# Performance work log

Measured on AMD Instinct MI355X. Metric: run time of the kernel, lower is better.

The kernel has to match this reference:

```python
import jax, jax.numpy as jnp
import numpy as np

B, T = 2048, 8
IN_DIM, OUT_DIM, E = 1024, 4096, 12


def setup_inputs() -> dict:
    key = jax.random.key(0)
    k = jax.random.split(key, 6)
    s = 1.0 / np.sqrt(IN_DIM)
    sg = 1.0 / np.sqrt(OUT_DIM)
    return {
        "x": jax.random.normal(k[0], (B, 1, IN_DIM), dtype=jnp.float32),
        "t": jax.random.normal(k[1], (B, T, OUT_DIM), dtype=jnp.float32),
        "W": jax.random.uniform(k[2], (E, IN_DIM, OUT_DIM), dtype=jnp.float32, minval=-s, maxval=s),
        "b": jax.random.uniform(k[3], (E, OUT_DIM), dtype=jnp.float32, minval=-s, maxval=s),
        "Wg": jax.random.uniform(k[4], (OUT_DIM, E), dtype=jnp.float32, minval=-sg, maxval=sg),
        "bg": jax.random.uniform(k[5], (E,), dtype=jnp.float32, minval=-sg, maxval=sg),
    }


def reference(x, t, W, b, Wg, bg):
    # x: [B,1,in], t: [B,T,out], W: [E,in,out], b: [E,out], Wg: [out,E], bg: [E]
    x_flat = x[:, 0, :]                                   # [B,in]
    t_mean = t.mean(axis=1)                               # [B,out]
    gate_logits = t_mean @ Wg + bg                        # [B,E]
    top1 = jnp.argmax(gate_logits, axis=-1)               # [B]
    # Dense per-expert linear, then select the top-1 expert's row per token.
    all_out = jnp.einsum('bi,eio->beo', x_flat, W) + b    # [B,E,out]
    out = all_out[jnp.arange(x.shape[0]), top1]           # [B,out]
    return out[:, None, :]                                # [B,1,out]
```

## Files before the change

### kernel.cpp

```cpp
#include <hip/hip_runtime.h>
#include <hip/hip_bf16.h>

#define B_ROWS  2048
#define T_DIM   8
#define IN_DIM  1024
#define OUT_DIM 4096
#define NE      12

#define M_TILE 128
#define N_TILE 128
#define K_STEP 32
#define NSTEP  (IN_DIM / K_STEP)

typedef __attribute__((ext_vector_type(8))) short short8;
typedef __attribute__((ext_vector_type(4))) float f32x4;

union S8U { short8 s; unsigned u[4]; };

__device__ __forceinline__ unsigned cvt2(float a, float b) {
  __hip_bfloat162 h = __float22bfloat162_rn(make_float2(a, b));
  union { __hip_bfloat162 h; unsigned u; } c; c.h = h;
  return c.u;
}

__device__ __forceinline__ void barrier_lgkm() {
  asm volatile("s_waitcnt lgkmcnt(0)" ::: "memory");
  __builtin_amdgcn_s_barrier();
}

__global__ __launch_bounds__(256) void wg_transpose(
    const float* __restrict__ Wg, float* __restrict__ wgt)
{
  const int c = blockIdx.x * 256 + threadIdx.x;
  #pragma unroll
  for (int e = 0; e < NE; ++e)
    wgt[(size_t)e * OUT_DIM + c] = Wg[(size_t)c * NE + e];
}

__global__ __launch_bounds__(256) void gate_kernel(
    const float* __restrict__ t, const float* __restrict__ wgt,
    const float* __restrict__ bg, int* __restrict__ counts,
    int* __restrict__ rowlist)
{
  const int b   = blockIdx.x;
  const int tid = threadIdx.x;
  const float* tb = t + (size_t)b * T_DIM * OUT_DIM;

  float4 m[4];
  #pragma unroll
  for (int it = 0; it < 4; ++it) {
    const int c = (tid + it * 256) * 4;
    float4 s = make_float4(0.f, 0.f, 0.f, 0.f);
    #pragma unroll
    for (int tt = 0; tt < T_DIM; ++tt) {
      const float4 v = *(const float4*)(tb + (size_t)tt * OUT_DIM + c);
      s.x += v.x; s.y += v.y; s.z += v.z; s.w += v.w;
    }
    m[it] = make_float4(s.x * 0.125f, s.y * 0.125f, s.z * 0.125f, s.w * 0.125f);
  }

  float part[NE];
  #pragma unroll
  for (int e = 0; e < NE; ++e) {
    float acc = 0.f;
    #pragma unroll
    for (int it = 0; it < 4; ++it) {
      const int c = (tid + it * 256) * 4;
      const float4 w = *(const float4*)(wgt + (size_t)e * OUT_DIM + c);
      acc += m[it].x * w.x; acc += m[it].y * w.y;
      acc += m[it].z * w.z; acc += m[it].w * w.w;
    }
    part[e] = acc;
  }

  double d[NE];
  #pragma unroll
  for (int e = 0; e < NE; ++e) d[e] = (double)part[e];
  #pragma unroll
  for (int off = 32; off > 0; off >>= 1) {
    #pragma unroll
    for (int e = 0; e < NE; ++e) d[e] += __shfl_down(d[e], off, 64);
  }

  __shared__ double wsred[4][NE];
  const int lane = tid & 63, wave = tid >> 6;
  if (lane == 0) {
    #pragma unroll
    for (int e = 0; e < NE; ++e) wsred[wave][e] = d[e];
  }
  __syncthreads();

  if (tid == 0) {
    double best = -1e300; int bi = 0;
    #pragma unroll
    for (int e = 0; e < NE; ++e) {
      const double v = wsred[0][e] + wsred[1][e] + wsred[2][e] + wsred[3][e] + (double)bg[e];
      if (v > best) { best = v; bi = e; }
    }
    const int pos = atomicAdd(&counts[bi], 1);
    rowlist[bi * B_ROWS + pos] = b;
  }
}

__global__ __launch_bounds__(256) void gate_fallback(
    const float* __restrict__ t, const float* __restrict__ Wg,
    const float* __restrict__ bg, int* __restrict__ counts,
    int* __restrict__ rowlist)
{
  const int b   = blockIdx.x;
  const int tid = threadIdx.x;
  const float* tb = t + (size_t)b * T_DIM * OUT_DIM;

  float part[NE];
  #pragma unroll
  for (int e = 0; e < NE; ++e) part[e] = 0.f;
  #pragma unroll
  for (int it = 0; it < 4; ++it) {
    const int c = (tid + it * 256) * 4;
    float4 s = make_float4(0.f, 0.f, 0.f, 0.f);
    #pragma unroll
    for (int tt = 0; tt < T_DIM; ++tt) {
      const float4 v = *(const float4*)(tb + (size_t)tt * OUT_DIM + c);
      s.x += v.x; s.y += v.y; s.z += v.z; s.w += v.w;
    }
    const float mm[4] = { s.x * 0.125f, s.y * 0.125f, s.z * 0.125f, s.w * 0.125f };
    #pragma unroll
    for (int j = 0; j < 4; ++j) {
      const float* wg = Wg + (size_t)(c + j) * NE;
      #pragma unroll
      for (int e = 0; e < NE; ++e) part[e] += mm[j] * wg[e];
    }
  }
  double d[NE];
  #pragma unroll
  for (int e = 0; e < NE; ++e) d[e] = (double)part[e];
  #pragma unroll
  for (int off = 32; off > 0; off >>= 1) {
    #pragma unroll
    for (int e = 0; e < NE; ++e) d[e] += __shfl_down(d[e], off, 64);
  }
  __shared__ double wsred[4][NE];
  const int lane = tid & 63, wave = tid >> 6;
  if (lane == 0) {
    #pragma unroll
    for (int e = 0; e < NE; ++e) wsred[wave][e] = d[e];
  }
  __syncthreads();
  if (tid == 0) {
    double best = -1e300; int bi = 0;
    #pragma unroll
    for (int e = 0; e < NE; ++e) {
      const double v = wsred[0][e] + wsred[1][e] + wsred[2][e] + wsred[3][e] + (double)bg[e];
      if (v > best) { best = v; bi = e; }
    }
    const int pos = atomicAdd(&counts[bi], 1);
    rowlist[bi * B_ROWS + pos] = b;
  }
}

__global__ __launch_bounds__(256) void expert_gemm(
    const float* __restrict__ x, const float* __restrict__ W,
    const float* __restrict__ bias, const int* __restrict__ counts,
    const int* __restrict__ rowlist, float* __restrict__ out)
{
  const int e    = blockIdx.z;
  const int cnt  = counts[e];
  const int row0 = blockIdx.y * M_TILE;
  if (row0 >= cnt) return;
  const int c0   = blockIdx.x * N_TILE;
  const int* rl  = rowlist + e * B_ROWS;

  __shared__ short8 xa[2][512];
  __shared__ short8 wb[2][512];

  const int tid  = threadIdx.x;
  const int lane = tid & 63;
  const int wave = tid >> 6;

  const int sg  = (tid >> 4) & 3;
  const int slr = tid & 15;
  const int smb = tid >> 6;

  int arow0, arow1;
  {
    const int g0 = row0 + smb * 16 + slr;
    const int g1 = row0 + (smb + 4) * 16 + slr;
    arow0 = rl[g0 < cnt ? g0 : cnt - 1];
    arow1 = rl[g1 < cnt ? g1 : cnt - 1];
  }
  const float* xp0 = x + (size_t)arow0 * IN_DIM + sg * 8;
  const float* xp1 = x + (size_t)arow1 * IN_DIM + sg * 8;
  const float* wp  = W + (size_t)e * IN_DIM * OUT_DIM
                       + (size_t)(sg * 8) * OUT_DIM + c0 + smb * 16 + slr;

  const int wm = (wave >> 1) * 64;
  const int wn = (wave & 1) * 64;
  const int abase = (wave >> 1) * 256;
  const int bbase = (wave & 1) * 256;

  f32x4 acc[4][4];
  #pragma unroll
  for (int m = 0; m < 4; ++m)
    #pragma unroll
    for (int n = 0; n < 4; ++n)
      #pragma unroll
      for (int q = 0; q < 4; ++q) acc[m][n][q] = 0.f;

  float4 a0lo, a0hi, a1lo, a1hi;
  float w0[8], w1[8];

#define ISSUE_LOADS(K)                                                  \
  {                                                                     \
    a0lo = *(const float4*)(xp0 + (K));                                 \
    a0hi = *(const float4*)(xp0 + (K) + 4);                             \
    a1lo = *(const float4*)(xp1 + (K));                                 \
    a1hi = *(const float4*)(xp1 + (K) + 4);                             \
    const float* p = wp + (size_t)(K) * OUT_DIM;                        \
    _Pragma("unroll")                                                   \
    for (int j = 0; j < 8; ++j) {                                       \
      w0[j] = p[(size_t)j * OUT_DIM];                                   \
      w1[j] = p[(size_t)j * OUT_DIM + 64];                              \
    }                                                                   \
  }

  ISSUE_LOADS(0);

  for (int it = 0; it < NSTEP; ++it) {
    S8U av0, av1, bv0, bv1;
    av0.u[0] = cvt2(a0lo.x, a0lo.y); av0.u[1] = cvt2(a0lo.z, a0lo.w);
    av0.u[2] = cvt2(a0hi.x, a0hi.y); av0.u[3] = cvt2(a0hi.z, a0hi.w);
    av1.u[0] = cvt2(a1lo.x, a1lo.y); av1.u[1] = cvt2(a1lo.z, a1lo.w);
    av1.u[2] = cvt2(a1hi.x, a1hi.y); av1.u[3] = cvt2(a1hi.z, a1hi.w);
    #pragma unroll
    for (int q = 0; q < 4; ++q) {
      bv0.u[q] = cvt2(w0[2 * q], w0[2 * q + 1]);
      bv1.u[q] = cvt2(w1[2 * q], w1[2 * q + 1]);
    }

    if (it + 1 < NSTEP) ISSUE_LOADS((it + 1) * K_STEP);

    const int buf = it & 1;
    xa[buf][tid]       = av0.s;
    xa[buf][tid + 256] = av1.s;
    wb[buf][tid]       = bv0.s;
    wb[buf][tid + 256] = bv1.s;
    barrier_lgkm();

    short8 af[4], bf[4];
    #pragma unroll
    for (int m = 0; m < 4; ++m) af[m] = xa[buf][abase + m * 64 + lane];
    #pragma unroll
    for (int n = 0; n < 4; ++n) bf[n] = wb[buf][bbase + n * 64 + lane];
    #pragma unroll
    for (int m = 0; m < 4; ++m)
      #pragma unroll
      for (int n = 0; n < 4; ++n)
        acc[m][n] = __builtin_amdgcn_mfma_f32_16x16x32_bf16(af[m], bf[n], acc[m][n], 0, 0, 0);
  }
#undef ISSUE_LOADS

  const int lr = lane & 15;
  const int lq = (lane >> 4) * 4;
  float bcol[4];
  #pragma unroll
  for (int n = 0; n < 4; ++n)
    bcol[n] = bias[e * OUT_DIM + c0 + wn + n * 16 + lr];

  #pragma unroll
  for (int m = 0; m < 4; ++m) {
    #pragma unroll
    for (int r = 0; r < 4; ++r) {
      const int gidx = row0 + wm + m * 16 + lq + r;
      if (gidx >= cnt) continue;
      const int grow = rl[gidx];
      float* orow = out + (size_t)grow * OUT_DIM;
      #pragma unroll
      for (int n = 0; n < 4; ++n) {
        const int col = c0 + wn + n * 16 + lr;
        orow[col] = acc[m][n][r] + bcol[n];
      }
    }
  }
}

extern "C" void kernel_launch(void* const* d_in, const int* in_sizes, int n_in,
                              void* d_out, int out_size, void* d_ws, size_t ws_size,
                              hipStream_t stream) {
  (void)in_sizes; (void)n_in; (void)out_size;
  const float* x  = (const float*)d_in[0];
  const float* t  = (const float*)d_in[1];
  const float* W  = (const float*)d_in[2];
  const float* bb = (const float*)d_in[3];
  const float* Wg = (const float*)d_in[4];
  const float* bg = (const float*)d_in[5];
  float* out = (float*)d_out;

  int*   counts  = (int*)d_ws;
  int*   rowlist = (int*)d_ws + 16;
  float* wgt     = (float*)((char*)d_ws + 64 + NE * B_ROWS * 4);
  const size_t need = 64 + (size_t)NE * B_ROWS * 4 + (size_t)NE * OUT_DIM * 4;

  hipMemsetAsync(counts, 0, 16 * sizeof(int), stream);
  if (ws_size >= need) {
    wg_transpose<<<OUT_DIM / 256, 256, 0, stream>>>(Wg, wgt);
    gate_kernel<<<B_ROWS, 256, 0, stream>>>(t, wgt, bg, counts, rowlist);
  } else {
    gate_fallback<<<B_ROWS, 256, 0, stream>>>(t, Wg, bg, counts, rowlist);
  }

  dim3 grid(OUT_DIM / N_TILE, (B_ROWS + M_TILE - 1) / M_TILE, NE);
  expert_gemm<<<grid, 256, 0, stream>>>(x, W, bb, counts, rowlist, out);
}
```

Measured before the change: 172.2 us.

## Split expert GEMM along K with atomic accumulation and bias pre-initialization

The expert GEMM is split four ways along the input dimension, so the grid has four times as many blocks, each running a quarter of the K loop. Partial sums are combined with float atomicAdd into the output. The output is first initialized with the selected expert's bias inside the gate kernel. The aim is more parallelism and better latency hiding in a GEMM that has few active tiles per expert. The cost is four atomic passes over the output, an extra full output write in the gate kernel, more per-block prologue overhead, and non-deterministic summation order.

```diff
diff --git a/kernel.cpp b/kernel.cpp
--- a/kernel.cpp
+++ b/kernel.cpp
@@ -11,6 +11,8 @@
 #define N_TILE 128
 #define K_STEP 32
 #define NSTEP  (IN_DIM / K_STEP)
+#define KSPLIT 4
+#define CSTEPS (NSTEP / KSPLIT)
 
 typedef __attribute__((ext_vector_type(8))) short short8;
 typedef __attribute__((ext_vector_type(4))) float f32x4;
@@ -39,8 +41,9 @@
 
 __global__ __launch_bounds__(256) void gate_kernel(
     const float* __restrict__ t, const float* __restrict__ wgt,
-    const float* __restrict__ bg, int* __restrict__ counts,
-    int* __restrict__ rowlist)
+    const float* __restrict__ bg, const float* __restrict__ bias,
+    int* __restrict__ counts, int* __restrict__ rowlist,
+    float* __restrict__ out)
 {
   const int b   = blockIdx.x;
   const int tid = threadIdx.x;
@@ -83,6 +86,7 @@
   }
 
   __shared__ double wsred[4][NE];
+  __shared__ int s_bi;
   const int lane = tid & 63, wave = tid >> 6;
   if (lane == 0) {
     #pragma unroll
@@ -99,13 +103,25 @@
     }
     const int pos = atomicAdd(&counts[bi], 1);
     rowlist[bi * B_ROWS + pos] = b;
+    s_bi = bi;
+  }
+  __syncthreads();
+
+  const int bi = s_bi;
+  const float* brow = bias + (size_t)bi * OUT_DIM;
+  float* orow = out + (size_t)b * OUT_DIM;
+  #pragma unroll
+  for (int it = 0; it < 4; ++it) {
+    const int c = (tid + it * 256) * 4;
+    *(float4*)(orow + c) = *(const float4*)(brow + c);
   }
 }
 
 __global__ __launch_bounds__(256) void gate_fallback(
     const float* __restrict__ t, const float* __restrict__ Wg,
-    const float* __restrict__ bg, int* __restrict__ counts,
-    int* __restrict__ rowlist)
+    const float* __restrict__ bg, const float* __restrict__ bias,
+    int* __restrict__ counts, int* __restrict__ rowlist,
+    float* __restrict__ out)
 {
   const int b   = blockIdx.x;
   const int tid = threadIdx.x;
@@ -140,6 +156,7 @@
     for (int e = 0; e < NE; ++e) d[e] += __shfl_down(d[e], off, 64);
   }
   __shared__ double wsred[4][NE];
+  __shared__ int s_bi;
   const int lane = tid & 63, wave = tid >> 6;
   if (lane == 0) {
     #pragma unroll
@@ -155,15 +172,26 @@
     }
     const int pos = atomicAdd(&counts[bi], 1);
     rowlist[bi * B_ROWS + pos] = b;
+    s_bi = bi;
+  }
+  __syncthreads();
+  const int bi = s_bi;
+  const float* brow = bias + (size_t)bi * OUT_DIM;
+  float* orow = out + (size_t)b * OUT_DIM;
+  #pragma unroll
+  for (int it = 0; it < 4; ++it) {
+    const int c = (tid + it * 256) * 4;
+    *(float4*)(orow + c) = *(const float4*)(brow + c);
   }
 }
 
 __global__ __launch_bounds__(256) void expert_gemm(
     const float* __restrict__ x, const float* __restrict__ W,
-    const float* __restrict__ bias, const int* __restrict__ counts,
-    const int* __restrict__ rowlist, float* __restrict__ out)
+    const int* __restrict__ counts, const int* __restrict__ rowlist,
+    float* __restrict__ out)
 {
-  const int e    = blockIdx.z;
+  const int e    = blockIdx.z / KSPLIT;
+  const int kc   = blockIdx.z % KSPLIT;
   const int cnt  = counts[e];
   const int row0 = blockIdx.y * M_TILE;
   if (row0 >= cnt) return;
@@ -223,9 +251,10 @@
     }                                                                   \
   }
 
-  ISSUE_LOADS(0);
-
-  for (int it = 0; it < NSTEP; ++it) {
+  const int it0 = kc * CSTEPS;
+  ISSUE_LOADS(it0 * K_STEP);
+
+  for (int it = it0; it < it0 + CSTEPS; ++it) {
     S8U av0, av1, bv0, bv1;
     av0.u[0] = cvt2(a0lo.x, a0lo.y); av0.u[1] = cvt2(a0lo.z, a0lo.w);
     av0.u[2] = cvt2(a0hi.x, a0hi.y); av0.u[3] = cvt2(a0hi.z, a0hi.w);
@@ -237,7 +266,7 @@
       bv1.u[q] = cvt2(w1[2 * q], w1[2 * q + 1]);
     }
 
-    if (it + 1 < NSTEP) ISSUE_LOADS((it + 1) * K_STEP);
+    if (it + 1 < it0 + CSTEPS) ISSUE_LOADS((it + 1) * K_STEP);
 
     const int buf = it & 1;
     xa[buf][tid]       = av0.s;
@@ -261,11 +290,6 @@
 
   const int lr = lane & 15;
   const int lq = (lane >> 4) * 4;
-  float bcol[4];
-  #pragma unroll
-  for (int n = 0; n < 4; ++n)
-    bcol[n] = bias[e * OUT_DIM + c0 + wn + n * 16 + lr];
-
   #pragma unroll
   for (int m = 0; m < 4; ++m) {
     #pragma unroll
@@ -277,7 +301,7 @@
       #pragma unroll
       for (int n = 0; n < 4; ++n) {
         const int col = c0 + wn + n * 16 + lr;
-        orow[col] = acc[m][n][r] + bcol[n];
+        atomicAdd(&orow[col], acc[m][n][r]);
       }
     }
   }
@@ -303,11 +327,11 @@
   hipMemsetAsync(counts, 0, 16 * sizeof(int), stream);
   if (ws_size >= need) {
     wg_transpose<<<OUT_DIM / 256, 256, 0, stream>>>(Wg, wgt);
-    gate_kernel<<<B_ROWS, 256, 0, stream>>>(t, wgt, bg, counts, rowlist);
+    gate_kernel<<<B_ROWS, 256, 0, stream>>>(t, wgt, bg, bb, counts, rowlist, out);
   } else {
-    gate_fallback<<<B_ROWS, 256, 0, stream>>>(t, Wg, bg, counts, rowlist);
-  }
-
-  dim3 grid(OUT_DIM / N_TILE, (B_ROWS + M_TILE - 1) / M_TILE, NE);
-  expert_gemm<<<grid, 256, 0, stream>>>(x, W, bb, counts, rowlist, out);
-}
+    gate_fallback<<<B_ROWS, 256, 0, stream>>>(t, Wg, bg, bb, counts, rowlist, out);
+  }
+
+  dim3 grid(OUT_DIM / N_TILE, (B_ROWS + M_TILE - 1) / M_TILE, NE * KSPLIT);
+  expert_gemm<<<grid, 256, 0, stream>>>(x, W, counts, rowlist, out);
+}
```

Measured after the change: 222.8 us. 1.29x slower.

## Double expert GEMM M tile to 256 and remap blocks for XCD locality

Applied to the files above, without the earlier changes.

Raises the expert GEMM row tile from 128 to 256. Each wave now computes a 64x128 output slab (acc 4x8), so every weight tile loaded from global is reused across twice as many token rows, which cuts W traffic. It also remaps the flattened block index so that neighbouring hardware dispatch slots map to the same expert and column range, aiming at better L2 sharing across XCDs. The cost is more accumulator registers (128 floats per lane) and therefore lower occupancy, plus coarser tail waste when an expert's token count is not a multiple of 256.

```diff
diff --git a/kernel.cpp b/kernel.cpp
--- a/kernel.cpp
+++ b/kernel.cpp
@@ -7,7 +7,7 @@
 #define OUT_DIM 4096
 #define NE      12
 
-#define M_TILE 128
+#define M_TILE 256
 #define N_TILE 128
 #define K_STEP 32
 #define NSTEP  (IN_DIM / K_STEP)
@@ -163,14 +163,16 @@
     const float* __restrict__ bias, const int* __restrict__ counts,
     const int* __restrict__ rowlist, float* __restrict__ out)
 {
-  const int e    = blockIdx.z;
+  const int bx = blockIdx.x;
+  const int gw = (bx & 7) * 48 + (bx >> 3) + 4 * blockIdx.z;
+  const int e  = gw >> 5;
+  const int c0 = (gw & 31) * N_TILE;
   const int cnt  = counts[e];
   const int row0 = blockIdx.y * M_TILE;
   if (row0 >= cnt) return;
-  const int c0   = blockIdx.x * N_TILE;
   const int* rl  = rowlist + e * B_ROWS;
 
-  __shared__ short8 xa[2][512];
+  __shared__ short8 xa[2][1024];
   __shared__ short8 wb[2][512];
 
   const int tid  = threadIdx.x;
@@ -181,40 +183,35 @@
   const int slr = tid & 15;
   const int smb = tid >> 6;
 
-  int arow0, arow1;
-  {
-    const int g0 = row0 + smb * 16 + slr;
-    const int g1 = row0 + (smb + 4) * 16 + slr;
-    arow0 = rl[g0 < cnt ? g0 : cnt - 1];
-    arow1 = rl[g1 < cnt ? g1 : cnt - 1];
-  }
-  const float* xp0 = x + (size_t)arow0 * IN_DIM + sg * 8;
-  const float* xp1 = x + (size_t)arow1 * IN_DIM + sg * 8;
-  const float* wp  = W + (size_t)e * IN_DIM * OUT_DIM
-                       + (size_t)(sg * 8) * OUT_DIM + c0 + smb * 16 + slr;
-
-  const int wm = (wave >> 1) * 64;
-  const int wn = (wave & 1) * 64;
-  const int abase = (wave >> 1) * 256;
-  const int bbase = (wave & 1) * 256;
-
-  f32x4 acc[4][4];
+  const float* xp[4];
+  #pragma unroll
+  for (int i = 0; i < 4; ++i) {
+    const int g = row0 + (smb + 4 * i) * 16 + slr;
+    xp[i] = x + (size_t)rl[g < cnt ? g : cnt - 1] * IN_DIM + sg * 8;
+  }
+  const float* wp = W + (size_t)e * IN_DIM * OUT_DIM
+                      + (size_t)(sg * 8) * OUT_DIM + c0 + smb * 16 + slr;
+
+  const int wm    = wave * 64;
+  const int abase = wave * 256;
+
+  f32x4 acc[4][8];
   #pragma unroll
   for (int m = 0; m < 4; ++m)
     #pragma unroll
-    for (int n = 0; n < 4; ++n)
+    for (int n = 0; n < 8; ++n)
       #pragma unroll
       for (int q = 0; q < 4; ++q) acc[m][n][q] = 0.f;
 
-  float4 a0lo, a0hi, a1lo, a1hi;
+  float4 axl0, axh0, axl1, axh1, axl2, axh2, axl3, axh3;
   float w0[8], w1[8];
 
 #define ISSUE_LOADS(K)                                                  \
   {                                                                     \
-    a0lo = *(const float4*)(xp0 + (K));                                 \
-    a0hi = *(const float4*)(xp0 + (K) + 4);                             \
-    a1lo = *(const float4*)(xp1 + (K));                                 \
-    a1hi = *(const float4*)(xp1 + (K) + 4);                             \
+    axl0 = *(const float4*)(xp[0] + (K)); axh0 = *(const float4*)(xp[0] + (K) + 4); \
+    axl1 = *(const float4*)(xp[1] + (K)); axh1 = *(const float4*)(xp[1] + (K) + 4); \
+    axl2 = *(const float4*)(xp[2] + (K)); axh2 = *(const float4*)(xp[2] + (K) + 4); \
+    axl3 = *(const float4*)(xp[3] + (K)); axh3 = *(const float4*)(xp[3] + (K) + 4); \
     const float* p = wp + (size_t)(K) * OUT_DIM;                        \
     _Pragma("unroll")                                                   \
     for (int j = 0; j < 8; ++j) {                                       \
@@ -226,11 +223,15 @@
   ISSUE_LOADS(0);
 
   for (int it = 0; it < NSTEP; ++it) {
-    S8U av0, av1, bv0, bv1;
-    av0.u[0] = cvt2(a0lo.x, a0lo.y); av0.u[1] = cvt2(a0lo.z, a0lo.w);
-    av0.u[2] = cvt2(a0hi.x, a0hi.y); av0.u[3] = cvt2(a0hi.z, a0hi.w);
-    av1.u[0] = cvt2(a1lo.x, a1lo.y); av1.u[1] = cvt2(a1lo.z, a1lo.w);
-    av1.u[2] = cvt2(a1hi.x, a1hi.y); av1.u[3] = cvt2(a1hi.z, a1hi.w);
+    S8U av0, av1, av2, av3, bv0, bv1;
+    av0.u[0] = cvt2(axl0.x, axl0.y); av0.u[1] = cvt2(axl0.z, axl0.w);
+    av0.u[2] = cvt2(axh0.x, axh0.y); av0.u[3] = cvt2(axh0.z, axh0.w);
+    av1.u[0] = cvt2(axl1.x, axl1.y); av1.u[1] = cvt2(axl1.z, axl1.w);
+    av1.u[2] = cvt2(axh1.x, axh1.y); av1.u[3] = cvt2(axh1.z, axh1.w);
+    av2.u[0] = cvt2(axl2.x, axl2.y); av2.u[1] = cvt2(axl2.z, axl2.w);
+    av2.u[2] = cvt2(axh2.x, axh2.y); av2.u[3] = cvt2(axh2.z, axh2.w);
+    av3.u[0] = cvt2(axl3.x, axl3.y); av3.u[1] = cvt2(axl3.z, axl3.w);
+    av3.u[2] = cvt2(axh3.x, axh3.y); av3.u[3] = cvt2(axh3.z, axh3.w);
     #pragma unroll
     for (int q = 0; q < 4; ++q) {
       bv0.u[q] = cvt2(w0[2 * q], w0[2 * q + 1]);
@@ -242,29 +243,31 @@
     const int buf = it & 1;
     xa[buf][tid]       = av0.s;
     xa[buf][tid + 256] = av1.s;
+    xa[buf][tid + 512] = av2.s;
+    xa[buf][tid + 768] = av3.s;
     wb[buf][tid]       = bv0.s;
     wb[buf][tid + 256] = bv1.s;
     barrier_lgkm();
 
-    short8 af[4], bf[4];
+    short8 af[4], bf[8];
     #pragma unroll
     for (int m = 0; m < 4; ++m) af[m] = xa[buf][abase + m * 64 + lane];
     #pragma unroll
-    for (int n = 0; n < 4; ++n) bf[n] = wb[buf][bbase + n * 64 + lane];
+    for (int n = 0; n < 8; ++n) bf[n] = wb[buf][n * 64 + lane];
     #pragma unroll
     for (int m = 0; m < 4; ++m)
       #pragma unroll
-      for (int n = 0; n < 4; ++n)
+      for (int n = 0; n < 8; ++n)
         acc[m][n] = __builtin_amdgcn_mfma_f32_16x16x32_bf16(af[m], bf[n], acc[m][n], 0, 0, 0);
   }
 #undef ISSUE_LOADS
 
   const int lr = lane & 15;
   const int lq = (lane >> 4) * 4;
-  float bcol[4];
-  #pragma unroll
-  for (int n = 0; n < 4; ++n)
-    bcol[n] = bias[e * OUT_DIM + c0 + wn + n * 16 + lr];
+  float bcol[8];
+  #pragma unroll
+  for (int n = 0; n < 8; ++n)
+    bcol[n] = bias[e * OUT_DIM + c0 + n * 16 + lr];
 
   #pragma unroll
   for (int m = 0; m < 4; ++m) {
@@ -275,8 +278,8 @@
       const int grow = rl[gidx];
       float* orow = out + (size_t)grow * OUT_DIM;
       #pragma unroll
-      for (int n = 0; n < 4; ++n) {
-        const int col = c0 + wn + n * 16 + lr;
+      for (int n = 0; n < 8; ++n) {
+        const int col = c0 + n * 16 + lr;
         orow[col] = acc[m][n][r] + bcol[n];
       }
     }
@@ -308,6 +311,6 @@
     gate_fallback<<<B_ROWS, 256, 0, stream>>>(t, Wg, bg, counts, rowlist);
   }
 
-  dim3 grid(OUT_DIM / N_TILE, (B_ROWS + M_TILE - 1) / M_TILE, NE);
+  dim3 grid(OUT_DIM / N_TILE, B_ROWS / M_TILE, NE);
   expert_gemm<<<grid, 256, 0, stream>>>(x, W, bb, counts, rowlist, out);
 }
```

Measured after the change: 181.2 us. 1.05x slower.

## Shrink GEMM N tile to 64 and remap blocks for XCD-aware scheduling

Applied to the files above, without the earlier changes.

Halves the expert GEMM column tile from 128 to 64. Each wave now computes a 32x64 slice instead of 64x64, which cuts accumulator registers and shared memory so that up to four blocks can share a CU (launch_bounds 256,4). Blocks are flattened into a 1D work index with an interleave over groups of 8, likely so that blocks on the same XCD share the same expert and weights in L2. Pairs of row tiles go along x so that launch order favours low row tiles. Smaller tiles mean more x reloads per W byte and less MFMA reuse per LDS load, in exchange for better occupancy and load balance across the uneven expert counts.

```diff
diff --git a/kernel.cpp b/kernel.cpp
--- a/kernel.cpp
+++ b/kernel.cpp
@@ -8,9 +8,10 @@
 #define NE      12
 
 #define M_TILE 128
-#define N_TILE 128
+#define N_TILE 64
 #define K_STEP 32
 #define NSTEP  (IN_DIM / K_STEP)
+#define NWORK  (NE * (OUT_DIM / N_TILE) * 2)
 
 typedef __attribute__((ext_vector_type(8))) short short8;
 typedef __attribute__((ext_vector_type(4))) float f32x4;
@@ -158,20 +159,24 @@
   }
 }
 
-__global__ __launch_bounds__(256) void expert_gemm(
+__global__ __launch_bounds__(256, 4) void expert_gemm(
     const float* __restrict__ x, const float* __restrict__ W,
     const float* __restrict__ bias, const int* __restrict__ counts,
     const int* __restrict__ rowlist, float* __restrict__ out)
 {
-  const int e    = blockIdx.z;
+  const int bid = blockIdx.x;
+  const int wk  = (bid & 7) * (NWORK / 8) + (bid >> 3);
+  const int e   = wk >> 7;
+  const int rem = wk & 127;
+  const int c0  = (rem >> 1) * N_TILE;
+  const int rt  = rem & 1;
   const int cnt  = counts[e];
-  const int row0 = blockIdx.y * M_TILE;
+  const int row0 = (blockIdx.y * 2 + rt) * M_TILE;
   if (row0 >= cnt) return;
-  const int c0   = blockIdx.x * N_TILE;
   const int* rl  = rowlist + e * B_ROWS;
 
   __shared__ short8 xa[2][512];
-  __shared__ short8 wb[2][512];
+  __shared__ short8 wb[2][256];
 
   const int tid  = threadIdx.x;
   const int lane = tid & 63;
@@ -193,21 +198,16 @@
   const float* wp  = W + (size_t)e * IN_DIM * OUT_DIM
                        + (size_t)(sg * 8) * OUT_DIM + c0 + smb * 16 + slr;
 
-  const int wm = (wave >> 1) * 64;
-  const int wn = (wave & 1) * 64;
-  const int abase = (wave >> 1) * 256;
-  const int bbase = (wave & 1) * 256;
-
-  f32x4 acc[4][4];
-  #pragma unroll
-  for (int m = 0; m < 4; ++m)
+  f32x4 acc[2][4];
+  #pragma unroll
+  for (int m = 0; m < 2; ++m)
     #pragma unroll
     for (int n = 0; n < 4; ++n)
       #pragma unroll
       for (int q = 0; q < 4; ++q) acc[m][n][q] = 0.f;
 
   float4 a0lo, a0hi, a1lo, a1hi;
-  float w0[8], w1[8];
+  float w0[8];
 
 #define ISSUE_LOADS(K)                                                  \
   {                                                                     \
@@ -217,25 +217,20 @@
     a1hi = *(const float4*)(xp1 + (K) + 4);                             \
     const float* p = wp + (size_t)(K) * OUT_DIM;                        \
     _Pragma("unroll")                                                   \
-    for (int j = 0; j < 8; ++j) {                                       \
-      w0[j] = p[(size_t)j * OUT_DIM];                                   \
-      w1[j] = p[(size_t)j * OUT_DIM + 64];                              \
-    }                                                                   \
+    for (int j = 0; j < 8; ++j) w0[j] = p[(size_t)j * OUT_DIM];         \
   }
 
   ISSUE_LOADS(0);
 
   for (int it = 0; it < NSTEP; ++it) {
-    S8U av0, av1, bv0, bv1;
+    S8U av0, av1, bv0;
     av0.u[0] = cvt2(a0lo.x, a0lo.y); av0.u[1] = cvt2(a0lo.z, a0lo.w);
     av0.u[2] = cvt2(a0hi.x, a0hi.y); av0.u[3] = cvt2(a0hi.z, a0hi.w);
     av1.u[0] = cvt2(a1lo.x, a1lo.y); av1.u[1] = cvt2(a1lo.z, a1lo.w);
     av1.u[2] = cvt2(a1hi.x, a1hi.y); av1.u[3] = cvt2(a1hi.z, a1hi.w);
     #pragma unroll
-    for (int q = 0; q < 4; ++q) {
+    for (int q = 0; q < 4; ++q)
       bv0.u[q] = cvt2(w0[2 * q], w0[2 * q + 1]);
-      bv1.u[q] = cvt2(w1[2 * q], w1[2 * q + 1]);
-    }
 
     if (it + 1 < NSTEP) ISSUE_LOADS((it + 1) * K_STEP);
 
@@ -243,16 +238,17 @@
     xa[buf][tid]       = av0.s;
     xa[buf][tid + 256] = av1.s;
     wb[buf][tid]       = bv0.s;
-    wb[buf][tid + 256] = bv1.s;
     barrier_lgkm();
 
-    short8 af[4], bf[4];
-    #pragma unroll
-    for (int m = 0; m < 4; ++m) af[m] = xa[buf][abase + m * 64 + lane];
-    #pragma unroll
-    for (int n = 0; n < 4; ++n) bf[n] = wb[buf][bbase + n * 64 + lane];
-    #pragma unroll
-    for (int m = 0; m < 4; ++m)
+    short8 af[2], bf[4];
+    #pragma unroll
+    for (int m = 0; m < 2; ++m)
+      af[m] = xa[buf][(2 * wave + m) * 64 + lane];
+    #pragma unroll
+    for (int n = 0; n < 4; ++n)
+      bf[n] = wb[buf][n * 64 + lane];
+    #pragma unroll
+    for (int m = 0; m < 2; ++m)
       #pragma unroll
       for (int n = 0; n < 4; ++n)
         acc[m][n] = __builtin_amdgcn_mfma_f32_16x16x32_bf16(af[m], bf[n], acc[m][n], 0, 0, 0);
@@ -264,19 +260,19 @@
   float bcol[4];
   #pragma unroll
   for (int n = 0; n < 4; ++n)
-    bcol[n] = bias[e * OUT_DIM + c0 + wn + n * 16 + lr];
-
-  #pragma unroll
-  for (int m = 0; m < 4; ++m) {
+    bcol[n] = bias[e * OUT_DIM + c0 + n * 16 + lr];
+
+  #pragma unroll
+  for (int m = 0; m < 2; ++m) {
     #pragma unroll
     for (int r = 0; r < 4; ++r) {
-      const int gidx = row0 + wm + m * 16 + lq + r;
+      const int gidx = row0 + wave * 32 + m * 16 + lq + r;
       if (gidx >= cnt) continue;
       const int grow = rl[gidx];
       float* orow = out + (size_t)grow * OUT_DIM;
       #pragma unroll
       for (int n = 0; n < 4; ++n) {
-        const int col = c0 + wn + n * 16 + lr;
+        const int col = c0 + n * 16 + lr;
         orow[col] = acc[m][n][r] + bcol[n];
       }
     }
@@ -308,6 +304,6 @@
     gate_fallback<<<B_ROWS, 256, 0, stream>>>(t, Wg, bg, counts, rowlist);
   }
 
-  dim3 grid(OUT_DIM / N_TILE, (B_ROWS + M_TILE - 1) / M_TILE, NE);
+  dim3 grid(NWORK, (B_ROWS / M_TILE) / 2, 1);
   expert_gemm<<<grid, 256, 0, stream>>>(x, W, bb, counts, rowlist, out);
 }
```

Measured after the change: 183.3 us. 6.4% more time.
